# Kernel tuning notes

Hardware: AMD Instinct MI355X
Metric: run time of the kernel (lower is better)

The kernel has to match this reference:

```python
import jax, jax.numpy as jnp
import numpy as np

B, N, D_IN, D_HID, D_OUT = 64, 512, 512, 512, 512


def setup_inputs() -> dict:
    key = jax.random.key(0)
    ks = jax.random.split(key, 8)
    gain = 0.02  # xavier_normal_ gain used in reset_parameters_xavier

    def xavier(k, fan_in, fan_out):
        std = gain * np.sqrt(2.0 / (fan_in + fan_out))
        return jax.random.normal(k, (fan_in, fan_out), dtype=jnp.float32) * std

    return {
        "batch_graph": jax.random.normal(ks[0], (B, N, D_IN), dtype=jnp.float32),
        "adj": jax.random.uniform(ks[1], (B, N, N), dtype=jnp.float32),
        "W1": xavier(ks[2], D_IN, D_HID),
        "b1": jnp.zeros((D_HID,), dtype=jnp.float32),
        "W2": xavier(ks[3], D_HID, D_HID),
        "b2": jnp.zeros((D_HID,), dtype=jnp.float32),
        "W3": xavier(ks[4], D_HID, D_OUT),
        "b3": jnp.zeros((D_OUT,), dtype=jnp.float32),
    }


def _normalize_adj(adj):
    # rowsum^-0.5 with inf -> 0 (original: torch.pow then isinf mask)
    rowsum = adj.sum(axis=1)                       # [B, N] (sum over dim 1, as in torch)
    safe = jnp.where(rowsum == 0, 1.0, rowsum)
    r = jnp.where(rowsum == 0, 0.0, safe ** -0.5)  # [B, N]
    # (adj @ D)^T @ D = D @ adj^T @ D with D = diag(r)
    return r[:, :, None] * jnp.swapaxes(adj, 1, 2) * r[:, None, :]


def reference(batch_graph, adj, W1, b1, W2, b2, W3, b3):
    # Block-diagonal big_adj @ big_graph == per-graph batched matmul.
    A = _normalize_adj(adj)  # [B, N, N]

    def gc(x, W, b):
        # support = x @ W ; output = A @ support + b
        return jnp.einsum('bij,bjd->bid', A, x @ W) + b

    # dropout is identity in eval mode (deterministic reference)
    x = jax.nn.relu(gc(batch_graph, W1, b1))
    x = jax.nn.relu(gc(x, W2, b2))
    return gc(x, W3, b3)  # [B, N, D_OUT]
```

## Files before the change

### kernel.cpp

```cpp
#include <hip/hip_runtime.h>
#include <cstdint>
#include <cstddef>

typedef _Float16 f16;
typedef _Float16 f16x4 __attribute__((ext_vector_type(4)));
typedef _Float16 f16x8 __attribute__((ext_vector_type(8)));
typedef float    f32x4 __attribute__((ext_vector_type(4)));

#define NB 64
#define NN 262144

__device__ __forceinline__ void gload_lds16(const void* g, void* l) {
    __builtin_amdgcn_global_load_lds(
        (const __attribute__((address_space(1))) void*)g,
        (__attribute__((address_space(3))) void*)l, 16, 0, 0);
}

__device__ __forceinline__ int SWC(int row, int col) {
    return ((((col >> 2) ^ (row >> 2)) & 15) << 2) | (col & 3);
}

__global__ __launch_bounds__(256)
void k_prep(const float* __restrict__ adj, f16* __restrict__ A_raw,
            float* __restrict__ part,
            const float* __restrict__ W1, const float* __restrict__ W2,
            const float* __restrict__ W3, f16* __restrict__ Wt,
            const float* __restrict__ X0, f16* __restrict__ Xa) {
    __shared__ __align__(16) float t[4096];
    __shared__ float red[4][64];
    const int bid = blockIdx.x, tid = threadIdx.x;

    bool do_cvt = false;
    int cvt_idx = 0;
    if (bid < 8192) {
        if (bid & 1) { do_cvt = true; cvt_idx = bid >> 1; }
    } else if (bid < 12288) {
        do_cvt = true; cvt_idx = 4096 + (bid - 8192);
    }

    if (do_cvt) {
        size_t i = ((size_t)cvt_idx * 256 + tid) * 8;
        float4 v0 = *(const float4*)(X0 + i);
        float4 v1 = *(const float4*)(X0 + i + 4);
        f16x8 o;
        o[0] = (f16)v0.x; o[1] = (f16)v0.y; o[2] = (f16)v0.z; o[3] = (f16)v0.w;
        o[4] = (f16)v1.x; o[5] = (f16)v1.y; o[6] = (f16)v1.z; o[7] = (f16)v1.w;
        *(f16x8*)(Xa + i) = o;
    } else if (bid < 8192) {
        const int idx = bid >> 1;
        const int xcd = idx & 7, loc = idx >> 3;
        const int b = xcd * 8 + (loc >> 6);
        const int tile = loc & 63;
        const int i0 = (tile >> 3) * 64, j0 = (tile & 7) * 64;
        const int jt = tile & 7;
        const float* ab = adj + (size_t)b * NN;
        #pragma unroll
        for (int s = 0; s < 4; ++s) {
            int rr = s * 16 + (tid >> 4);
            int creal = SWC(rr, (tid & 15) * 4);
            gload_lds16(&ab[(size_t)(j0 + rr) * 512 + i0 + creal],
                        &t[s * 1024 + tid * 4]);
        }
        asm volatile("s_waitcnt vmcnt(0)" ::: "memory");
        __syncthreads();
        {
            int c = tid & 63, g = tid >> 6;
            float sg = 0.f;
            #pragma unroll
            for (int s = 0; s < 16; ++s) {
                int row = g * 16 + s;
                sg += t[row * 64 + SWC(row, c)];
            }
            red[g][c] = sg;
        }
        f16* Ab = A_raw + (size_t)b * NN;
        int jq = (tid & 15) * 4;
        int ib = tid >> 4;
        #pragma unroll
        for (int s = 0; s < 4; ++s) {
            int ii = ib + s * 16;
            f16x4 o;
            #pragma unroll
            for (int q = 0; q < 4; ++q)
                o[q] = (f16)t[(jq + q) * 64 + SWC(jq + q, ii)];
            *(f16x4*)&Ab[(size_t)(i0 + ii) * 512 + j0 + jq] = o;
        }
        __syncthreads();
        if (tid < 64)
            part[((size_t)b * 8 + jt) * 512 + i0 + tid] =
                red[0][tid] + red[1][tid] + red[2][tid] + red[3][tid];
    } else {
        int cb = bid - 12288;
        int z = cb >> 6, rem = cb & 63;
        const float* W = z == 0 ? W1 : (z == 1 ? W2 : W3);
        f16* out = Wt + (size_t)z * NN;
        int k0 = (rem >> 3) * 64, d0 = (rem & 7) * 64;
        int c = tid & 63, r4 = tid >> 6;
        #pragma unroll
        for (int s = 0; s < 16; ++s) {
            int rr = r4 + s * 4;
            t[rr * 64 + SWC(rr, c)] = W[(size_t)(k0 + rr) * 512 + d0 + c];
        }
        __syncthreads();
        int kq = (tid & 15) * 4;
        int db = tid >> 4;
        #pragma unroll
        for (int s = 0; s < 4; ++s) {
            int dd = db + s * 16;
            f16x4 o;
            #pragma unroll
            for (int q = 0; q < 4; ++q)
                o[q] = (f16)(64.f * t[(kq + q) * 64 + SWC(kq + q, dd)]);
            *(f16x4*)&out[(size_t)(d0 + dd) * 512 + k0 + kq] = o;
        }
    }
}

template<bool BIAS, bool RELU, bool OUTF32, bool RM, bool RN>
__global__ __launch_bounds__(256, 2)
void gemm_tn_ct(const f16* __restrict__ P, size_t pstr,
                const f16* __restrict__ Qt, size_t qstr,
                void* __restrict__ Cout, size_t cstr,
                const float* __restrict__ bias, const float* __restrict__ part,
                float iscale, float oscale) {
    __shared__ __align__(16) f16 Plds[2][8192];
    __shared__ __align__(16) f16 Qlds[2][8192];
    __shared__ float rs_lds[128];

    const int tid  = threadIdx.x;
    const int lane = tid & 63;
    const int wid  = tid >> 6;
    const int wm   = wid >> 1;
    const int wn   = wid & 1;

    const int wg  = blockIdx.x;
    const int swz = (wg & 7) * 128 + (wg >> 3);
    const int b   = swz >> 4;
    const int tt  = swz & 15;
    const int m0  = (tt >> 2) * 128;
    const int n0  = (tt & 3) * 128;

    const f16* Pb = P + (size_t)b * pstr;
    const f16* Qb = Qt + (size_t)b * qstr;

    const int srow = tid >> 3;
    const int sswz = (tid & 7) ^ (srow & 7);

    const int fr  = lane & 15;
    const int fs  = lane >> 4;
    const int fx  = fr & 7;

    auto stage = [&](const f16* __restrict__ Gb, int row0, f16* lds, int k0) {
        #pragma unroll
        for (int r = 0; r < 4; ++r) {
            const f16* src = Gb + (size_t)(row0 + r * 32 + srow) * 512 + k0 + sswz * 8;
            gload_lds16(src, lds + r * 2048 + tid * 8);
        }
    };

    f32x4 acc[4][4] = {};

    stage(Pb, m0, &Plds[0][0], 0);
    stage(Qb, n0, &Qlds[0][0], 0);

    if ((RM || RN) && tid < 128) {
        const float* p = part + (size_t)b * 4096 + (RM ? m0 : n0) + tid;
        float s = 0.f;
        #pragma unroll
        for (int jt = 0; jt < 8; ++jt) s += p[jt * 512];
        rs_lds[tid] = (s > 0.f) ? rsqrtf(s) : 0.f;
    }

    for (int t = 0; t < 8; ++t) {
        const int nb = t & 1;
        if (t < 7) {
            stage(Pb, m0, &Plds[nb ^ 1][0], (t + 1) * 64);
            stage(Qb, n0, &Qlds[nb ^ 1][0], (t + 1) * 64);
            asm volatile("s_waitcnt vmcnt(8)" ::: "memory");
        } else {
            asm volatile("s_waitcnt vmcnt(0)" ::: "memory");
        }
        __builtin_amdgcn_s_barrier();

        const f16* Pl = &Plds[nb][0];
        const f16* Ql = &Qlds[nb][0];
        #pragma unroll
        for (int krep = 0; krep < 2; ++krep) {
            const int sp = ((fs + krep * 4) ^ fx) * 8;
            f16x8 af[4], bf[4];
            #pragma unroll
            for (int mi = 0; mi < 4; ++mi)
                af[mi] = *(const f16x8*)&Pl[(wm * 64 + mi * 16 + fr) * 64 + sp];
            #pragma unroll
            for (int ni = 0; ni < 4; ++ni)
                bf[ni] = *(const f16x8*)&Ql[(wn * 64 + ni * 16 + fr) * 64 + sp];
            __builtin_amdgcn_s_setprio(1);
            #pragma unroll
            for (int mi = 0; mi < 4; ++mi)
                #pragma unroll
                for (int ni = 0; ni < 4; ++ni)
                    acc[mi][ni] = __builtin_amdgcn_mfma_f32_16x16x32_f16(
                        af[mi], bf[ni], acc[mi][ni], 0, 0, 0);
            __builtin_amdgcn_s_setprio(0);
        }
        asm volatile("s_waitcnt lgkmcnt(0)" ::: "memory");
        __builtin_amdgcn_sched_barrier(0);
        __builtin_amdgcn_s_barrier();
    }

    const int cmb = (lane >> 4) * 4;
    f32x4 rm4[4];
    float rn1[4];
    if (RM) {
        #pragma unroll
        for (int mi = 0; mi < 4; ++mi)
            rm4[mi] = *(const f32x4*)&rs_lds[wm * 64 + mi * 16 + cmb];
    }
    if (RN) {
        #pragma unroll
        for (int ni = 0; ni < 4; ++ni)
            rn1[ni] = rs_lds[wn * 64 + ni * 16 + fr];
    }
    #pragma unroll
    for (int mi = 0; mi < 4; ++mi) {
        #pragma unroll
        for (int ni = 0; ni < 4; ++ni) {
            const int n = n0 + wn * 64 + ni * 16 + fr;
            const int m = m0 + wm * 64 + mi * 16 + cmb;
            float v[4];
            #pragma unroll
            for (int q = 0; q < 4; ++q) {
                float x = acc[mi][ni][q] * iscale;
                if (RM) x *= rm4[mi][q];
                if (RN) x *= rn1[ni];
                if (BIAS) x += bias[m + q];
                if (RELU) x = fmaxf(x, 0.f);
                v[q] = x * oscale;
            }
            if (OUTF32) {
                float* Cb = (float*)Cout + (size_t)b * cstr;
                f32x4 o; o[0] = v[0]; o[1] = v[1]; o[2] = v[2]; o[3] = v[3];
                *(f32x4*)&Cb[(size_t)n * 512 + m] = o;
            } else {
                f16* Cb = (f16*)Cout + (size_t)b * cstr;
                f16x4 o; o[0] = (f16)v[0]; o[1] = (f16)v[1]; o[2] = (f16)v[2]; o[3] = (f16)v[3];
                *(f16x4*)&Cb[(size_t)n * 512 + m] = o;
            }
        }
    }
}

extern "C" void kernel_launch(void* const* d_in, const int* in_sizes, int n_in,
                              void* d_out, int out_size, void* d_ws, size_t ws_size,
                              hipStream_t stream) {
    const float* X0  = (const float*)d_in[0];
    const float* adj = (const float*)d_in[1];
    const float* W1  = (const float*)d_in[2];
    const float* b1  = (const float*)d_in[3];
    const float* W2  = (const float*)d_in[4];
    const float* b2  = (const float*)d_in[5];
    const float* W3  = (const float*)d_in[6];
    const float* b3  = (const float*)d_in[7];

    uint8_t* ws = (uint8_t*)d_ws;
    float* part = (float*)ws;
    f16* Wt1 = (f16*)(ws + (1 << 20));
    f16* A_raw = (f16*)(ws + (1 << 20) + (size_t)3 * NN * 2);
    f16* Xa  = A_raw + (size_t)NB * NN;
    f16* S_t = Xa + (size_t)NB * NN;

    k_prep<<<dim3(12480), dim3(256), 0, stream>>>(adj, A_raw, part, W1, W2, W3, Wt1, X0, Xa);

    dim3 gg(1024), gb(256);
    gemm_tn_ct<false, false, false, true,  false><<<gg, gb, 0, stream>>>(Xa,  (size_t)NN, Wt1, (size_t)0,  S_t, (size_t)NN, nullptr, part, 4.f, 1.f);
    gemm_tn_ct<true,  true,  false, false, true ><<<gg, gb, 0, stream>>>(S_t, (size_t)NN, A_raw, (size_t)NN, Xa, (size_t)NN, b1, part, 1.f / 256.f, 256.f);
    gemm_tn_ct<false, false, false, true,  false><<<gg, gb, 0, stream>>>(Xa,  (size_t)NN, Wt1 + NN, (size_t)0,  S_t, (size_t)NN, nullptr, part, 16.f, 1.f);
    gemm_tn_ct<true,  true,  false, false, true ><<<gg, gb, 0, stream>>>(S_t, (size_t)NN, A_raw, (size_t)NN, Xa, (size_t)NN, b2, part, 1.f / 262144.f, 256.f);
    gemm_tn_ct<false, false, false, true,  false><<<gg, gb, 0, stream>>>(Xa,  (size_t)NN, Wt1 + 2 * NN, (size_t)0,  S_t, (size_t)NN, nullptr, part, 16.f, 1.f);
    gemm_tn_ct<true,  false, true,  false, true ><<<gg, gb, 0, stream>>>(S_t, (size_t)NN, A_raw, (size_t)NN, d_out, (size_t)NN, b3, part, 1.f / 262144.f, 1.f);
}
```

Baseline: 215.9 us.

## Use 256x256 tiles with 8 waves and interleaved four-phase load/MFMA schedule

Replaces the 128x128, 4-wave GEMM with a 256x256 tile handled by 512 threads (8 waves, each computing 128x64). Each K step is split into four phases that interleave LDS fragment loads, global-to-LDS prefetch of half-tiles and MFMA blocks, with barriers between them. The larger tile roughly halves global/L2 traffic per flop and overlaps prefetch with compute. In exchange it runs only 256 workgroups (one per CU at 1 block/CU), uses 128KB of LDS, adds more barriers, and puts more pressure on accumulator registers.

New measurement: 200.9 us (median of 2 runs). 1.07x faster.

```diff
diff --git a/kernel.cpp b/kernel.cpp
--- a/kernel.cpp
+++ b/kernel.cpp
@@ -117,104 +117,128 @@
 }
 
 template<bool BIAS, bool RELU, bool OUTF32, bool RM, bool RN>
-__global__ __launch_bounds__(256, 2)
-void gemm_tn_ct(const f16* __restrict__ P, size_t pstr,
-                const f16* __restrict__ Qt, size_t qstr,
-                void* __restrict__ Cout, size_t cstr,
-                const float* __restrict__ bias, const float* __restrict__ part,
-                float iscale, float oscale) {
-    __shared__ __align__(16) f16 Plds[2][8192];
-    __shared__ __align__(16) f16 Qlds[2][8192];
-    __shared__ float rs_lds[128];
+__global__ __launch_bounds__(512, 1)
+void gemm8(const f16* __restrict__ P, size_t pstr,
+           const f16* __restrict__ Qt, size_t qstr,
+           void* __restrict__ Cout, size_t cstr,
+           const float* __restrict__ bias, const float* __restrict__ part,
+           float iscale, float oscale) {
+    __shared__ __align__(16) f16 Albuf[2][16384];
+    __shared__ __align__(16) f16 Blbuf[2][16384];
+    __shared__ float rs_lds[256];
 
     const int tid  = threadIdx.x;
     const int lane = tid & 63;
     const int wid  = tid >> 6;
-    const int wm   = wid >> 1;
-    const int wn   = wid & 1;
+    const int wm   = wid >> 2;
+    const int wn   = wid & 3;
 
     const int wg  = blockIdx.x;
-    const int swz = (wg & 7) * 128 + (wg >> 3);
-    const int b   = swz >> 4;
-    const int tt  = swz & 15;
-    const int m0  = (tt >> 2) * 128;
-    const int n0  = (tt & 3) * 128;
+    const int swz = (wg & 7) * 32 + (wg >> 3);
+    const int b   = swz >> 2;
+    const int tt  = swz & 3;
+    const int m0  = (tt >> 1) * 256;
+    const int n0  = (tt & 1) * 256;
 
     const f16* Pb = P + (size_t)b * pstr;
     const f16* Qb = Qt + (size_t)b * qstr;
 
-    const int srow = tid >> 3;
-    const int sswz = (tid & 7) ^ (srow & 7);
-
-    const int fr  = lane & 15;
-    const int fs  = lane >> 4;
-    const int fx  = fr & 7;
-
-    auto stage = [&](const f16* __restrict__ Gb, int row0, f16* lds, int k0) {
-        #pragma unroll
-        for (int r = 0; r < 4; ++r) {
-            const f16* src = Gb + (size_t)(row0 + r * 32 + srow) * 512 + k0 + sswz * 8;
-            gload_lds16(src, lds + r * 2048 + tid * 8);
-        }
-    };
-
-    f32x4 acc[4][4] = {};
-
-    stage(Pb, m0, &Plds[0][0], 0);
-    stage(Qb, n0, &Qlds[0][0], 0);
-
-    if ((RM || RN) && tid < 128) {
+    const int fr = lane & 15, fs = lane >> 4, fx = fr & 7;
+
+    if ((RM || RN) && tid < 256) {
         const float* p = part + (size_t)b * 4096 + (RM ? m0 : n0) + tid;
         float s = 0.f;
         #pragma unroll
         for (int jt = 0; jt < 8; ++jt) s += p[jt * 512];
         rs_lds[tid] = (s > 0.f) ? rsqrtf(s) : 0.f;
     }
+    asm volatile("s_waitcnt vmcnt(0)" ::: "memory");
+
+    auto stage_half = [&](const f16* __restrict__ Gb, int row0g, f16* buf, int h, int k0) {
+        {
+            int row = tid >> 3, sl = tid & 7;
+            gload_lds16(Gb + (size_t)(row0g + h * 128 + row) * 512 + k0 + ((sl ^ (row & 7)) * 8),
+                        buf + h * 8192 + tid * 8);
+        }
+        {
+            int u = tid + 512;
+            int row = u >> 3, sl = u & 7;
+            gload_lds16(Gb + (size_t)(row0g + h * 128 + row) * 512 + k0 + ((sl ^ (row & 7)) * 8),
+                        buf + h * 8192 + u * 8);
+        }
+    };
+
+    f32x4 acc[8][4] = {};
+    f16x8 af[4][2], bf[2][2];
+
+    stage_half(Qb, n0, &Blbuf[0][0], 0, 0);
+    stage_half(Qb, n0, &Blbuf[0][0], 1, 0);
+    stage_half(Pb, m0, &Albuf[0][0], 0, 0);
+    stage_half(Pb, m0, &Albuf[0][0], 1, 0);
+
+#define LOAD_AF(QM)                                                            \
+    _Pragma("unroll") for (int i = 0; i < 4; ++i) {                            \
+        int row = wm * 128 + ((QM) * 4 + i) * 16 + fr;                         \
+        _Pragma("unroll") for (int k = 0; k < 2; ++k)                          \
+            af[i][k] = *(const f16x8*)&Al[row * 64 + ((fs + 4 * k) ^ fx) * 8]; \
+    }
+#define LOAD_BF(QN)                                                            \
+    _Pragma("unroll") for (int j = 0; j < 2; ++j) {                            \
+        int row = wn * 64 + ((QN) * 2 + j) * 16 + fr;                          \
+        _Pragma("unroll") for (int k = 0; k < 2; ++k)                          \
+            bf[j][k] = *(const f16x8*)&Bl[row * 64 + ((fs + 4 * k) ^ fx) * 8]; \
+    }
+#define PH_SYNC()                                                              \
+    __builtin_amdgcn_s_barrier();                                              \
+    asm volatile("s_waitcnt lgkmcnt(0)" ::: "memory");                         \
+    __builtin_amdgcn_sched_barrier(0);
+#define DO_MFMA(QM, QN)                                                        \
+    __builtin_amdgcn_s_setprio(1);                                             \
+    _Pragma("unroll") for (int i = 0; i < 4; ++i)                              \
+        _Pragma("unroll") for (int j = 0; j < 2; ++j)                          \
+            _Pragma("unroll") for (int k = 0; k < 2; ++k)                      \
+                acc[(QM) * 4 + i][(QN) * 2 + j] =                              \
+                    __builtin_amdgcn_mfma_f32_16x16x32_f16(                    \
+                        af[i][k], bf[j][k], acc[(QM) * 4 + i][(QN) * 2 + j],   \
+                        0, 0, 0);                                              \
+    __builtin_amdgcn_s_setprio(0);                                             \
+    __builtin_amdgcn_s_barrier();
 
     for (int t = 0; t < 8; ++t) {
-        const int nb = t & 1;
-        if (t < 7) {
-            stage(Pb, m0, &Plds[nb ^ 1][0], (t + 1) * 64);
-            stage(Qb, n0, &Qlds[nb ^ 1][0], (t + 1) * 64);
-            asm volatile("s_waitcnt vmcnt(8)" ::: "memory");
-        } else {
-            asm volatile("s_waitcnt vmcnt(0)" ::: "memory");
-        }
+        f16* Al = &Albuf[t & 1][0];
+        f16* Bl = &Blbuf[t & 1][0];
+        f16* An = &Albuf[(t & 1) ^ 1][0];
+        f16* Bn = &Blbuf[(t & 1) ^ 1][0];
+        const int kn = (t + 1) * 64;
+
+        asm volatile("s_waitcnt vmcnt(0)" ::: "memory");
         __builtin_amdgcn_s_barrier();
 
-        const f16* Pl = &Plds[nb][0];
-        const f16* Ql = &Qlds[nb][0];
-        #pragma unroll
-        for (int krep = 0; krep < 2; ++krep) {
-            const int sp = ((fs + krep * 4) ^ fx) * 8;
-            f16x8 af[4], bf[4];
-            #pragma unroll
-            for (int mi = 0; mi < 4; ++mi)
-                af[mi] = *(const f16x8*)&Pl[(wm * 64 + mi * 16 + fr) * 64 + sp];
-            #pragma unroll
-            for (int ni = 0; ni < 4; ++ni)
-                bf[ni] = *(const f16x8*)&Ql[(wn * 64 + ni * 16 + fr) * 64 + sp];
-            __builtin_amdgcn_s_setprio(1);
-            #pragma unroll
-            for (int mi = 0; mi < 4; ++mi)
-                #pragma unroll
-                for (int ni = 0; ni < 4; ++ni)
-                    acc[mi][ni] = __builtin_amdgcn_mfma_f32_16x16x32_f16(
-                        af[mi], bf[ni], acc[mi][ni], 0, 0, 0);
-            __builtin_amdgcn_s_setprio(0);
-        }
-        asm volatile("s_waitcnt lgkmcnt(0)" ::: "memory");
-        __builtin_amdgcn_sched_barrier(0);
-        __builtin_amdgcn_s_barrier();
-    }
+        LOAD_AF(0) LOAD_BF(0)
+        if (t < 7) stage_half(Qb, n0, Bn, 0, kn);
+        PH_SYNC(); DO_MFMA(0, 0)
+        LOAD_BF(1)
+        if (t < 7) stage_half(Qb, n0, Bn, 1, kn);
+        PH_SYNC(); DO_MFMA(0, 1)
+        LOAD_AF(1)
+        if (t < 7) stage_half(Pb, m0, An, 0, kn);
+        PH_SYNC(); DO_MFMA(1, 1)
+        LOAD_BF(0)
+        if (t < 7) stage_half(Pb, m0, An, 1, kn);
+        PH_SYNC(); DO_MFMA(1, 0)
+    }
+#undef LOAD_AF
+#undef LOAD_BF
+#undef PH_SYNC
+#undef DO_MFMA
 
     const int cmb = (lane >> 4) * 4;
-    f32x4 rm4[4];
+    f32x4 rm4[8];
     float rn1[4];
     if (RM) {
         #pragma unroll
-        for (int mi = 0; mi < 4; ++mi)
-            rm4[mi] = *(const f32x4*)&rs_lds[wm * 64 + mi * 16 + cmb];
+        for (int mi = 0; mi < 8; ++mi)
+            rm4[mi] = *(const f32x4*)&rs_lds[wm * 128 + mi * 16 + cmb];
     }
     if (RN) {
         #pragma unroll
@@ -222,11 +246,11 @@
             rn1[ni] = rs_lds[wn * 64 + ni * 16 + fr];
     }
     #pragma unroll
-    for (int mi = 0; mi < 4; ++mi) {
+    for (int mi = 0; mi < 8; ++mi) {
         #pragma unroll
         for (int ni = 0; ni < 4; ++ni) {
             const int n = n0 + wn * 64 + ni * 16 + fr;
-            const int m = m0 + wm * 64 + mi * 16 + cmb;
+            const int m = m0 + wm * 128 + mi * 16 + cmb;
             float v[4];
             #pragma unroll
             for (int q = 0; q < 4; ++q) {
@@ -271,11 +295,11 @@
 
     k_prep<<<dim3(12480), dim3(256), 0, stream>>>(adj, A_raw, part, W1, W2, W3, Wt1, X0, Xa);
 
-    dim3 gg(1024), gb(256);
-    gemm_tn_ct<false, false, false, true,  false><<<gg, gb, 0, stream>>>(Xa,  (size_t)NN, Wt1, (size_t)0,  S_t, (size_t)NN, nullptr, part, 4.f, 1.f);
-    gemm_tn_ct<true,  true,  false, false, true ><<<gg, gb, 0, stream>>>(S_t, (size_t)NN, A_raw, (size_t)NN, Xa, (size_t)NN, b1, part, 1.f / 256.f, 256.f);
-    gemm_tn_ct<false, false, false, true,  false><<<gg, gb, 0, stream>>>(Xa,  (size_t)NN, Wt1 + NN, (size_t)0,  S_t, (size_t)NN, nullptr, part, 16.f, 1.f);
-    gemm_tn_ct<true,  true,  false, false, true ><<<gg, gb, 0, stream>>>(S_t, (size_t)NN, A_raw, (size_t)NN, Xa, (size_t)NN, b2, part, 1.f / 262144.f, 256.f);
-    gemm_tn_ct<false, false, false, true,  false><<<gg, gb, 0, stream>>>(Xa,  (size_t)NN, Wt1 + 2 * NN, (size_t)0,  S_t, (size_t)NN, nullptr, part, 16.f, 1.f);
-    gemm_tn_ct<true,  false, true,  false, true ><<<gg, gb, 0, stream>>>(S_t, (size_t)NN, A_raw, (size_t)NN, d_out, (size_t)NN, b3, part, 1.f / 262144.f, 1.f);
-}
+    dim3 gg(256), gb(512);
+    gemm8<false, false, false, true,  false><<<gg, gb, 0, stream>>>(Xa,  (size_t)NN, Wt1, (size_t)0,  S_t, (size_t)NN, nullptr, part, 4.f, 1.f);
+    gemm8<true,  true,  false, false, true ><<<gg, gb, 0, stream>>>(S_t, (size_t)NN, A_raw, (size_t)NN, Xa, (size_t)NN, b1, part, 1.f / 256.f, 256.f);
+    gemm8<false, false, false, true,  false><<<gg, gb, 0, stream>>>(Xa,  (size_t)NN, Wt1 + NN, (size_t)0,  S_t, (size_t)NN, nullptr, part, 16.f, 1.f);
+    gemm8<true,  true,  false, false, true ><<<gg, gb, 0, stream>>>(S_t, (size_t)NN, A_raw, (size_t)NN, Xa, (size_t)NN, b2, part, 1.f / 262144.f, 256.f);
+    gemm8<false, false, false, true,  false><<<gg, gb, 0, stream>>>(Xa,  (size_t)NN, Wt1 + 2 * NN, (size_t)0,  S_t, (size_t)NN, nullptr, part, 16.f, 1.f);
+    gemm8<true,  false, true,  false, true ><<<gg, gb, 0, stream>>>(S_t, (size_t)NN, A_raw, (size_t)NN, d_out, (size_t)NN, b3, part, 1.f / 262144.f, 1.f);
+}
```
